# Performance work log

Measured on AMD Instinct MI355X. Metric: run time of the kernel, lower is better.

The kernel has to match this reference:

```python
import jax, jax.numpy as jnp
import numpy as np

N = 16384          # num nodes (adj is dense NxN)
INPUT_DIM = 512
HIDDEN = 128
E_POS = 524288
E_NEG = 524288


def setup_inputs() -> dict:
    key = jax.random.key(0)
    k1, k2, k3, k4, k5, k6, k7 = jax.random.split(key, 7)
    X = jax.random.normal(k1, (N, INPUT_DIM), dtype=jnp.float32)
    adj = jax.random.uniform(k2, (N, N), dtype=jnp.float32)
    train_edges = jax.random.randint(k3, (E_POS, 2), 0, N, dtype=jnp.int64)
    train_false_edges = jax.random.randint(k4, (E_NEG, 2), 0, N, dtype=jnp.int64)
    # parameters (xavier / kaiming scale approximated with uniform bounds)
    b1 = float(np.sqrt(6.0 / (INPUT_DIM + HIDDEN)))
    weight = jax.random.uniform(k5, (INPUT_DIM, HIDDEN), minval=-b1, maxval=b1, dtype=jnp.float32)
    b2 = float(np.sqrt(6.0 / (2 * HIDDEN + HIDDEN)))
    weight_two = jax.random.uniform(k6, (2 * HIDDEN, HIDDEN), minval=-b2, maxval=b2, dtype=jnp.float32)
    b3 = float(np.sqrt(6.0 / HIDDEN) / np.sqrt(2.0))  # kaiming_uniform a=1
    weight_three = jax.random.uniform(k7, (HIDDEN, 1), minval=-b3, maxval=b3, dtype=jnp.float32)
    return {"X": X, "adj": adj, "weight": weight, "weight_two": weight_two,
            "weight_three": weight_three, "train_edges": train_edges,
            "train_false_edges": train_false_edges}


def reference(X, adj, weight, weight_two, weight_three, train_edges, train_false_edges):
    # encode: Z = adj @ (X @ W)
    Z = adj @ (X @ weight)                                  # [N, H]
    edges = jnp.concatenate([train_edges, train_false_edges], axis=0)  # [E, 2]
    # decode: vectorized gather-concat replacing the per-edge Python loop
    z_pair = jnp.concatenate([Z[edges[:, 0]], Z[edges[:, 1]]], axis=1)  # [E, 2H]
    h = jax.nn.relu(z_pair) @ weight_two @ weight_three      # [E, 1]
    return jax.nn.sigmoid(h)
```

## Files before the change

### kernel.cpp

```cpp
#include <hip/hip_runtime.h>


#define N_NODES 16384
#define IN_DIM  512
#define HID     128
#define E_POS_N 524288
#define E_TOT   1048576

typedef __bf16 bf16x8 __attribute__((ext_vector_type(8)));
typedef float  f32x4  __attribute__((ext_vector_type(4)));
typedef unsigned short us8 __attribute__((ext_vector_type(8)));

__device__ __forceinline__ bf16x8 ldsb(const void* p){
  return __builtin_bit_cast(bf16x8, *reinterpret_cast<const us8*>(p));
}
__device__ __forceinline__ void gload16(const void* g, void* l){
  __builtin_amdgcn_global_load_lds(
      (const __attribute__((address_space(1))) unsigned int*)g,
      (__attribute__((address_space(3))) unsigned int*)l, 16, 0, 0);
}

__device__ __forceinline__ void split8(const float* f, bf16x8& hi, bf16x8& lo){
  unsigned short h[8];
  __bf16 l[8];
#pragma unroll
  for (int i = 0; i < 8; ++i){
    unsigned u  = __float_as_uint(f[i]);
    unsigned hb = u & 0xFFFF0000u;
    h[i] = (unsigned short)(hb >> 16);
    l[i] = (__bf16)(f[i] - __uint_as_float(hb));
  }
  us8 hv = {h[0], h[1], h[2], h[3], h[4], h[5], h[6], h[7]};
  hi = __builtin_bit_cast(bf16x8, hv);
  bf16x8 lv = {l[0], l[1], l[2], l[3], l[4], l[5], l[6], l[7]};
  lo = lv;
}

__global__ __launch_bounds__(256) void xw_kernel(const float* __restrict__ X,
                                                 const float* __restrict__ W,
                                                 unsigned short* __restrict__ bfB){
  __shared__ float Xt[32][64];
  __shared__ float Ws[32][128];
  const int tid = threadIdx.x;
  const int m0  = blockIdx.x * 64;
  const int ty  = tid >> 5;
  const int tx  = tid & 31;
  const int sr  = tid >> 2;
  const int sq  = tid & 3;
  const int wk  = tid >> 3;
  const int wc  = (tid & 7) * 16;
  float acc[8][4] = {};
  for (int kt = 0; kt < 16; ++kt){
    const int k0 = kt * 32;
    __syncthreads();
    {
      const float* xp = X + (size_t)(m0 + sr) * IN_DIM + k0 + sq * 8;
      float4 x0 = *(const float4*)xp;
      float4 x1 = *(const float4*)(xp + 4);
      Xt[sq*8+0][sr] = x0.x; Xt[sq*8+1][sr] = x0.y; Xt[sq*8+2][sr] = x0.z; Xt[sq*8+3][sr] = x0.w;
      Xt[sq*8+4][sr] = x1.x; Xt[sq*8+5][sr] = x1.y; Xt[sq*8+6][sr] = x1.z; Xt[sq*8+7][sr] = x1.w;
      const float* wp = W + (size_t)(k0 + wk) * HID + wc;
      *(float4*)&Ws[wk][wc+0]  = *(const float4*)(wp + 0);
      *(float4*)&Ws[wk][wc+4]  = *(const float4*)(wp + 4);
      *(float4*)&Ws[wk][wc+8]  = *(const float4*)(wp + 8);
      *(float4*)&Ws[wk][wc+12] = *(const float4*)(wp + 12);
    }
    __syncthreads();
#pragma unroll 8
    for (int kk = 0; kk < 32; ++kk){
      float4 a0 = *(const float4*)&Xt[kk][ty*8];
      float4 a1 = *(const float4*)&Xt[kk][ty*8+4];
      float4 b  = *(const float4*)&Ws[kk][tx*4];
      float av[8] = {a0.x,a0.y,a0.z,a0.w,a1.x,a1.y,a1.z,a1.w};
      float bv[4] = {b.x,b.y,b.z,b.w};
#pragma unroll
      for (int i = 0; i < 8; ++i)
#pragma unroll
        for (int c = 0; c < 4; ++c)
          acc[i][c] = fmaf(av[i], bv[c], acc[i][c]);
    }
  }
  const int row0 = m0 + ty * 8;
  const int tile = row0 >> 5;
  const int g    = (row0 >> 3) & 3;
#pragma unroll
  for (int cc = 0; cc < 4; ++cc){
    const int c  = tx * 4 + cc;
    const int sw = (c & 7) << 4;
    float f[8];
#pragma unroll
    for (int i = 0; i < 8; ++i) f[i] = acc[i][cc];
    bf16x8 hi, lo; split8(f, hi, lo);
    char* tb = (char*)bfB + (size_t)tile * 16384 + (size_t)c * 128;
    *(us8*)(tb + ((g * 16) ^ sw))      = __builtin_bit_cast(us8, hi);
    *(us8*)(tb + ((64 + g * 16) ^ sw)) = __builtin_bit_cast(us8, lo);
  }
}

__global__ void w23_kernel(const float* __restrict__ w2, const float* __restrict__ w3,
                           float* __restrict__ w23){
  const int t = threadIdx.x;
  float acc = 0.f;
#pragma unroll 4
  for (int k = 0; k < HID; ++k) acc = fmaf(w2[t * HID + k], w3[k], acc);
  w23[t] = acc;
}

__global__ __launch_bounds__(512, 2) void zgemm_kernel(const float* __restrict__ adj,
                                                       const unsigned short* __restrict__ bfB,
                                                       float* __restrict__ part,
                                                       int ksplit){
  __shared__ alignas(16) char lds[3][49152];
  const int tid  = threadIdx.x;
  const int lane = tid & 63;
  const int w    = tid >> 6;
  const int wm   = w >> 1;
  const int wn   = w & 1;
  int mt, s;
  if (ksplit == 4){
    const int xcd = blockIdx.x & 7, idx = blockIdx.x >> 3;
    s = xcd & 3; mt = ((xcd >> 2) << 5) + idx;
  } else { mt = blockIdx.x & 63; s = blockIdx.x >> 6; }
  const int klen = N_NODES / ksplit;
  const int k0   = s * klen;
  const int nt   = klen >> 5;

  const int g = lane >> 4, l15 = lane & 15;
  int aoff[4][2], boffH[4], boffL[4];
#pragma unroll
  for (int m = 0; m < 4; ++m){
    const int r = wm * 64 + m * 16 + l15;
    const int sw = (r & 7) << 4;
    aoff[m][0] = r * 128 + ((g * 32) ^ sw);
    aoff[m][1] = r * 128 + ((g * 32 + 16) ^ sw);
  }
#pragma unroll
  for (int n = 0; n < 4; ++n){
    const int c = wn * 64 + n * 16 + l15;
    const int sw = (c & 7) << 4;
    boffH[n] = 32768 + c * 128 + ((g * 16) ^ sw);
    boffL[n] = 32768 + c * 128 + ((64 + g * 16) ^ sw);
  }

  const char* asrc[4]; int aldo[4];
#pragma unroll
  for (int c4 = 0; c4 < 4; ++c4){
    const int r = c4 * 64 + (tid >> 3);
    asrc[c4] = (const char*)adj + ((size_t)(mt * 256 + r) * N_NODES + k0) * 4
               + (((tid & 7) * 16) ^ ((r & 7) << 4));
    aldo[c4] = c4 * 8192 + tid * 16;
  }
  const char* bsrc = (const char*)bfB + (size_t)(k0 >> 5) * 16384 + tid * 16;

#define STAGE(buf, tt) do { \
    _Pragma("unroll") \
    for (int c4 = 0; c4 < 4; ++c4) \
      gload16(asrc[c4] + (size_t)(tt) * 128, (buf) + aldo[c4]); \
    gload16(bsrc + (size_t)(tt) * 16384,        (buf) + 32768 + tid * 16); \
    gload16(bsrc + (size_t)(tt) * 16384 + 8192, (buf) + 40960 + tid * 16); \
  } while (0)

  f32x4 acc[4][4] = {};

  auto compute = [&](const char* bp){
    bf16x8 bHv[4], bLv[4];
#pragma unroll
    for (int n = 0; n < 4; ++n){
      bHv[n] = ldsb(bp + boffH[n]);
      bLv[n] = ldsb(bp + boffL[n]);
    }
#pragma unroll
    for (int m = 0; m < 4; ++m){
      f32x4 v0 = *(const f32x4*)(bp + aoff[m][0]);
      f32x4 v1 = *(const f32x4*)(bp + aoff[m][1]);
      float f[8] = {v0[0], v0[1], v0[2], v0[3], v1[0], v1[1], v1[2], v1[3]};
      bf16x8 aH, aL; split8(f, aH, aL);
      __builtin_amdgcn_s_setprio(1);
#pragma unroll
      for (int n = 0; n < 4; ++n)
        acc[m][n] = __builtin_amdgcn_mfma_f32_16x16x32_bf16(aH, bHv[n], acc[m][n], 0, 0, 0);
#pragma unroll
      for (int n = 0; n < 4; ++n)
        acc[m][n] = __builtin_amdgcn_mfma_f32_16x16x32_bf16(aH, bLv[n], acc[m][n], 0, 0, 0);
#pragma unroll
      for (int n = 0; n < 4; ++n)
        acc[m][n] = __builtin_amdgcn_mfma_f32_16x16x32_bf16(aL, bHv[n], acc[m][n], 0, 0, 0);
      __builtin_amdgcn_s_setprio(0);
    }
  };

  char* pc = lds[0]; char* pn = lds[1]; char* pf = lds[2];
  STAGE(pc, 0);
  STAGE(pn, 1);
  asm volatile("s_waitcnt vmcnt(6)" ::: "memory");
  __builtin_amdgcn_s_barrier();
  asm volatile("" ::: "memory");

  for (int t = 0; t < nt; ++t){
    if (t + 2 < nt) STAGE(pf, t + 2);
    compute(pc);
    if (t + 2 < nt)      asm volatile("s_waitcnt vmcnt(6)" ::: "memory");
    else if (t + 1 < nt) asm volatile("s_waitcnt vmcnt(0)" ::: "memory");
    if (t + 1 < nt){
      __builtin_amdgcn_s_barrier();
      asm volatile("" ::: "memory");
    }
    char* tmp = pc; pc = pn; pn = pf; pf = tmp;
  }
#undef STAGE

  float* pb = part + (size_t)s * ((size_t)N_NODES * HID);
  const int row0 = mt * 256 + wm * 64;
  const int col0 = wn * 64;
#pragma unroll
  for (int m = 0; m < 4; ++m){
#pragma unroll
    for (int n = 0; n < 4; ++n){
#pragma unroll
      for (int j = 0; j < 4; ++j){
        const int row = row0 + m * 16 + (lane >> 4) * 4 + j;
        const int col = col0 + n * 16 + l15;
        pb[(size_t)row * HID + col] = acc[m][n][j];
      }
    }
  }
}

__global__ __launch_bounds__(256) void nodered_kernel(const float* __restrict__ part,
                                                      const float* __restrict__ w23,
                                                      float* __restrict__ aarr,
                                                      float* __restrict__ barr,
                                                      int ksplit){
  const int lane = threadIdx.x & 63;
  const int wv   = threadIdx.x >> 6;
  const int n    = blockIdx.x * 4 + wv;
  const float* p = part + (size_t)n * HID;
  float z1 = 0.f, z2 = 0.f;
  for (int s = 0; s < ksplit; ++s){
    const size_t o = (size_t)s * N_NODES * HID;
    z1 += p[o + lane];
    z2 += p[o + lane + 64];
  }
  z1 = fmaxf(z1, 0.f); z2 = fmaxf(z2, 0.f);
  float av = z1 * w23[lane]       + z2 * w23[lane + 64];
  float bv = z1 * w23[128 + lane] + z2 * w23[192 + lane];
#pragma unroll
  for (int o = 32; o > 0; o >>= 1){
    av += __shfl_down(av, o);
    bv += __shfl_down(bv, o);
  }
  if (lane == 0){ aarr[n] = av; barr[n] = bv; }
}

__global__ __launch_bounds__(256) void edge_kernel(const int* __restrict__ e0,
                                                   const int* __restrict__ e1,
                                                   const float* __restrict__ aarr,
                                                   const float* __restrict__ barr,
                                                   float* __restrict__ out){
  const int e = blockIdx.x * 256 + threadIdx.x;
  int i, j;
  if (e < E_POS_N){ i = e0[2 * e];  j = e0[2 * e + 1]; }
  else { const int ee = e - E_POS_N; i = e1[2 * ee]; j = e1[2 * ee + 1]; }
  const float h = aarr[i] + barr[j];
  out[e] = 1.0f / (1.0f + __expf(-h));
}

extern "C" void kernel_launch(void* const* d_in, const int* in_sizes, int n_in,
                              void* d_out, int out_size, void* d_ws, size_t ws_size,
                              hipStream_t stream){
  const float* X   = (const float*)d_in[0];
  const float* adj = (const float*)d_in[1];
  const float* W   = (const float*)d_in[2];
  const float* W2  = (const float*)d_in[3];
  const float* W3  = (const float*)d_in[4];
  const int*   e0  = (const int*)d_in[5];
  const int*   e1  = (const int*)d_in[6];
  float* out = (float*)d_out;

  char* wsb = (char*)d_ws;
  unsigned short* bfB = (unsigned short*)(wsb);
  float* w23  = (float*)(wsb + (size_t)8 * 1024 * 1024);
  float* aarr = (float*)(wsb + (size_t)8 * 1024 * 1024 + 65536);
  float* barr = (float*)(wsb + (size_t)8 * 1024 * 1024 + 2 * 65536);
  float* part = (float*)(wsb + (size_t)16 * 1024 * 1024);

  const size_t PART = (size_t)N_NODES * HID * 4;
  const size_t base = (size_t)16 * 1024 * 1024;
  int ksplit = 1;
  if (ws_size >= base + 4 * PART) ksplit = 4;
  else if (ws_size >= base + 2 * PART) ksplit = 2;

  hipLaunchKernelGGL(xw_kernel, dim3(N_NODES / 64), dim3(256), 0, stream, X, W, bfB);
  hipLaunchKernelGGL(w23_kernel, dim3(1), dim3(256), 0, stream, W2, W3, w23);
  hipLaunchKernelGGL(zgemm_kernel, dim3(64 * ksplit), dim3(512), 0, stream,
                     adj, bfB, part, ksplit);
  hipLaunchKernelGGL(nodered_kernel, dim3(N_NODES / 4), dim3(256), 0, stream,
                     part, w23, aarr, barr, ksplit);
  hipLaunchKernelGGL(edge_kernel, dim3(E_TOT / 256), dim3(256), 0, stream,
                     e0, e1, aarr, barr, out);
}
```

Before: 312.4 us.

## Retile adjacency GEMM, move X@W to split-bf16 MFMA, vectorize edge and reduction kernels

The adjacency GEMM now uses 128-row tiles with a fixed 2-way K split, 4-stage LDS buffering and a different XCD mapping. The old dynamic ksplit selection based on workspace size is removed. X@W moves from scalar FMA to the same split-bf16 MFMA pipeline, fed by a new prep kernel that pre-splits W and also computes w23. split8 now uses byte-perm instructions. The node reduction handles four nodes per wave, and the edge kernel processes four edges per thread with vector loads and stores. Smaller GEMM tiles reduce reuse of B per adj load and change occupancy; the fixed split also assumes the workspace can hold two partial buffers.

```diff
diff --git a/kernel.cpp b/kernel.cpp
--- a/kernel.cpp
+++ b/kernel.cpp
@@ -10,6 +10,7 @@
 typedef __bf16 bf16x8 __attribute__((ext_vector_type(8)));
 typedef float  f32x4  __attribute__((ext_vector_type(4)));
 typedef unsigned short us8 __attribute__((ext_vector_type(8)));
+typedef unsigned short us4 __attribute__((ext_vector_type(4)));
 
 __device__ __forceinline__ bf16x8 ldsb(const void* p){
   return __builtin_bit_cast(bf16x8, *reinterpret_cast<const us8*>(p));
@@ -21,154 +22,91 @@
 }
 
 __device__ __forceinline__ void split8(const float* f, bf16x8& hi, bf16x8& lo){
-  unsigned short h[8];
-  __bf16 l[8];
-#pragma unroll
-  for (int i = 0; i < 8; ++i){
-    unsigned u  = __float_as_uint(f[i]);
-    unsigned hb = u & 0xFFFF0000u;
-    h[i] = (unsigned short)(hb >> 16);
-    l[i] = (__bf16)(f[i] - __uint_as_float(hb));
-  }
-  us8 hv = {h[0], h[1], h[2], h[3], h[4], h[5], h[6], h[7]};
+  unsigned u[8];
+#pragma unroll
+  for (int i = 0; i < 8; ++i) u[i] = __float_as_uint(f[i]);
+  uint4 hv;
+  hv.x = __builtin_amdgcn_perm(u[1], u[0], 0x07060302u);
+  hv.y = __builtin_amdgcn_perm(u[3], u[2], 0x07060302u);
+  hv.z = __builtin_amdgcn_perm(u[5], u[4], 0x07060302u);
+  hv.w = __builtin_amdgcn_perm(u[7], u[6], 0x07060302u);
   hi = __builtin_bit_cast(bf16x8, hv);
-  bf16x8 lv = {l[0], l[1], l[2], l[3], l[4], l[5], l[6], l[7]};
+  bf16x8 lv;
+#pragma unroll
+  for (int i = 0; i < 8; ++i)
+    lv[i] = (__bf16)(f[i] - __uint_as_float(u[i] & 0xFFFF0000u));
   lo = lv;
 }
 
-__global__ __launch_bounds__(256) void xw_kernel(const float* __restrict__ X,
-                                                 const float* __restrict__ W,
-                                                 unsigned short* __restrict__ bfB){
-  __shared__ float Xt[32][64];
-  __shared__ float Ws[32][128];
-  const int tid = threadIdx.x;
-  const int m0  = blockIdx.x * 64;
-  const int ty  = tid >> 5;
-  const int tx  = tid & 31;
-  const int sr  = tid >> 2;
-  const int sq  = tid & 3;
-  const int wk  = tid >> 3;
-  const int wc  = (tid & 7) * 16;
-  float acc[8][4] = {};
-  for (int kt = 0; kt < 16; ++kt){
-    const int k0 = kt * 32;
-    __syncthreads();
-    {
-      const float* xp = X + (size_t)(m0 + sr) * IN_DIM + k0 + sq * 8;
-      float4 x0 = *(const float4*)xp;
-      float4 x1 = *(const float4*)(xp + 4);
-      Xt[sq*8+0][sr] = x0.x; Xt[sq*8+1][sr] = x0.y; Xt[sq*8+2][sr] = x0.z; Xt[sq*8+3][sr] = x0.w;
-      Xt[sq*8+4][sr] = x1.x; Xt[sq*8+5][sr] = x1.y; Xt[sq*8+6][sr] = x1.z; Xt[sq*8+7][sr] = x1.w;
-      const float* wp = W + (size_t)(k0 + wk) * HID + wc;
-      *(float4*)&Ws[wk][wc+0]  = *(const float4*)(wp + 0);
-      *(float4*)&Ws[wk][wc+4]  = *(const float4*)(wp + 4);
-      *(float4*)&Ws[wk][wc+8]  = *(const float4*)(wp + 8);
-      *(float4*)&Ws[wk][wc+12] = *(const float4*)(wp + 12);
-    }
-    __syncthreads();
-#pragma unroll 8
-    for (int kk = 0; kk < 32; ++kk){
-      float4 a0 = *(const float4*)&Xt[kk][ty*8];
-      float4 a1 = *(const float4*)&Xt[kk][ty*8+4];
-      float4 b  = *(const float4*)&Ws[kk][tx*4];
-      float av[8] = {a0.x,a0.y,a0.z,a0.w,a1.x,a1.y,a1.z,a1.w};
-      float bv[4] = {b.x,b.y,b.z,b.w};
-#pragma unroll
-      for (int i = 0; i < 8; ++i)
-#pragma unroll
-        for (int c = 0; c < 4; ++c)
-          acc[i][c] = fmaf(av[i], bv[c], acc[i][c]);
-    }
-  }
-  const int row0 = m0 + ty * 8;
-  const int tile = row0 >> 5;
-  const int g    = (row0 >> 3) & 3;
-#pragma unroll
-  for (int cc = 0; cc < 4; ++cc){
-    const int c  = tx * 4 + cc;
+__global__ __launch_bounds__(512) void prep_kernel(const float* __restrict__ W,
+                                                   const float* __restrict__ w2,
+                                                   const float* __restrict__ w3,
+                                                   unsigned short* __restrict__ bfW,
+                                                   float* __restrict__ w23){
+  const int blk = blockIdx.x, tid = threadIdx.x;
+  if (blk < 16){
+    const int c = tid & 127, g = tid >> 7;
+    float f[8];
+#pragma unroll
+    for (int j = 0; j < 8; ++j) f[j] = W[(blk * 32 + g * 8 + j) * HID + c];
+    bf16x8 hi, lo; split8(f, hi, lo);
     const int sw = (c & 7) << 4;
-    float f[8];
-#pragma unroll
-    for (int i = 0; i < 8; ++i) f[i] = acc[i][cc];
-    bf16x8 hi, lo; split8(f, hi, lo);
-    char* tb = (char*)bfB + (size_t)tile * 16384 + (size_t)c * 128;
+    char* tb = (char*)bfW + blk * 16384 + c * 128;
     *(us8*)(tb + ((g * 16) ^ sw))      = __builtin_bit_cast(us8, hi);
     *(us8*)(tb + ((64 + g * 16) ^ sw)) = __builtin_bit_cast(us8, lo);
-  }
-}
-
-__global__ void w23_kernel(const float* __restrict__ w2, const float* __restrict__ w3,
-                           float* __restrict__ w23){
-  const int t = threadIdx.x;
-  float acc = 0.f;
+  } else if (tid < 256){
+    float acc = 0.f;
 #pragma unroll 4
-  for (int k = 0; k < HID; ++k) acc = fmaf(w2[t * HID + k], w3[k], acc);
-  w23[t] = acc;
-}
-
-__global__ __launch_bounds__(512, 2) void zgemm_kernel(const float* __restrict__ adj,
-                                                       const unsigned short* __restrict__ bfB,
-                                                       float* __restrict__ part,
-                                                       int ksplit){
-  __shared__ alignas(16) char lds[3][49152];
-  const int tid  = threadIdx.x;
-  const int lane = tid & 63;
-  const int w    = tid >> 6;
-  const int wm   = w >> 1;
-  const int wn   = w & 1;
-  int mt, s;
-  if (ksplit == 4){
-    const int xcd = blockIdx.x & 7, idx = blockIdx.x >> 3;
-    s = xcd & 3; mt = ((xcd >> 2) << 5) + idx;
-  } else { mt = blockIdx.x & 63; s = blockIdx.x >> 6; }
-  const int klen = N_NODES / ksplit;
-  const int k0   = s * klen;
-  const int nt   = klen >> 5;
-
+    for (int k = 0; k < HID; ++k) acc = fmaf(w2[tid * HID + k], w3[k], acc);
+    w23[tid] = acc;
+  }
+}
+
+__global__ __launch_bounds__(256) void xw_kernel(const float* __restrict__ X,
+                                                 const unsigned short* __restrict__ bfW,
+                                                 unsigned short* __restrict__ bfB){
+  __shared__ alignas(16) char lds[4][24576];
+  const int tid = threadIdx.x, lane = tid & 63, w = tid >> 6;
+  const int blk = blockIdx.x;
   const int g = lane >> 4, l15 = lane & 15;
-  int aoff[4][2], boffH[4], boffL[4];
+
+  int aoff[4][2], boffH[2], boffL[2];
 #pragma unroll
   for (int m = 0; m < 4; ++m){
-    const int r = wm * 64 + m * 16 + l15;
-    const int sw = (r & 7) << 4;
+    const int r = m * 16 + l15, sw = (r & 7) << 4;
     aoff[m][0] = r * 128 + ((g * 32) ^ sw);
     aoff[m][1] = r * 128 + ((g * 32 + 16) ^ sw);
   }
 #pragma unroll
-  for (int n = 0; n < 4; ++n){
-    const int c = wn * 64 + n * 16 + l15;
-    const int sw = (c & 7) << 4;
-    boffH[n] = 32768 + c * 128 + ((g * 16) ^ sw);
-    boffL[n] = 32768 + c * 128 + ((64 + g * 16) ^ sw);
-  }
-
-  const char* asrc[4]; int aldo[4];
-#pragma unroll
-  for (int c4 = 0; c4 < 4; ++c4){
-    const int r = c4 * 64 + (tid >> 3);
-    asrc[c4] = (const char*)adj + ((size_t)(mt * 256 + r) * N_NODES + k0) * 4
-               + (((tid & 7) * 16) ^ ((r & 7) << 4));
-    aldo[c4] = c4 * 8192 + tid * 16;
-  }
-  const char* bsrc = (const char*)bfB + (size_t)(k0 >> 5) * 16384 + tid * 16;
-
-#define STAGE(buf, tt) do { \
-    _Pragma("unroll") \
-    for (int c4 = 0; c4 < 4; ++c4) \
-      gload16(asrc[c4] + (size_t)(tt) * 128, (buf) + aldo[c4]); \
-    gload16(bsrc + (size_t)(tt) * 16384,        (buf) + 32768 + tid * 16); \
-    gload16(bsrc + (size_t)(tt) * 16384 + 8192, (buf) + 40960 + tid * 16); \
+  for (int n = 0; n < 2; ++n){
+    const int c = (w & 3) * 32 + n * 16 + l15, sw = (c & 7) << 4;
+    boffH[n] = 8192 + c * 128 + ((g * 16) ^ sw);
+    boffL[n] = 8192 + c * 128 + ((64 + g * 16) ^ sw);
+  }
+
+  const char* xsrc[2];
+#pragma unroll
+  for (int i = 0; i < 2; ++i){
+    const int r = i * 32 + (tid >> 3);
+    xsrc[i] = (const char*)X + ((size_t)(blk * 64 + r) * IN_DIM) * 4
+            + (((tid & 7) * 16) ^ ((r & 7) << 4));
+  }
+  const char* bsrc = (const char*)bfW + tid * 16;
+
+#define XSTAGE(buf, tt) do { \
+    gload16(xsrc[0] + (tt) * 128, (buf) + tid * 16); \
+    gload16(xsrc[1] + (tt) * 128, (buf) + 4096 + tid * 16); \
+    gload16(bsrc + (size_t)(tt) * 16384,         (buf) + 8192  + tid * 16); \
+    gload16(bsrc + (size_t)(tt) * 16384 + 4096,  (buf) + 12288 + tid * 16); \
+    gload16(bsrc + (size_t)(tt) * 16384 + 8192,  (buf) + 16384 + tid * 16); \
+    gload16(bsrc + (size_t)(tt) * 16384 + 12288, (buf) + 20480 + tid * 16); \
   } while (0)
 
-  f32x4 acc[4][4] = {};
-
+  f32x4 acc[4][2] = {};
   auto compute = [&](const char* bp){
-    bf16x8 bHv[4], bLv[4];
-#pragma unroll
-    for (int n = 0; n < 4; ++n){
-      bHv[n] = ldsb(bp + boffH[n]);
-      bLv[n] = ldsb(bp + boffL[n]);
-    }
+    bf16x8 bHv[2], bLv[2];
+#pragma unroll
+    for (int n = 0; n < 2; ++n){ bHv[n] = ldsb(bp + boffH[n]); bLv[n] = ldsb(bp + boffL[n]); }
 #pragma unroll
     for (int m = 0; m < 4; ++m){
       f32x4 v0 = *(const f32x4*)(bp + aoff[m][0]);
@@ -177,48 +115,148 @@
       bf16x8 aH, aL; split8(f, aH, aL);
       __builtin_amdgcn_s_setprio(1);
 #pragma unroll
-      for (int n = 0; n < 4; ++n)
-        acc[m][n] = __builtin_amdgcn_mfma_f32_16x16x32_bf16(aH, bHv[n], acc[m][n], 0, 0, 0);
-#pragma unroll
-      for (int n = 0; n < 4; ++n)
-        acc[m][n] = __builtin_amdgcn_mfma_f32_16x16x32_bf16(aH, bLv[n], acc[m][n], 0, 0, 0);
-#pragma unroll
-      for (int n = 0; n < 4; ++n)
-        acc[m][n] = __builtin_amdgcn_mfma_f32_16x16x32_bf16(aL, bHv[n], acc[m][n], 0, 0, 0);
+      for (int n = 0; n < 2; ++n) acc[m][n] = __builtin_amdgcn_mfma_f32_16x16x32_bf16(aH, bHv[n], acc[m][n], 0, 0, 0);
+#pragma unroll
+      for (int n = 0; n < 2; ++n) acc[m][n] = __builtin_amdgcn_mfma_f32_16x16x32_bf16(aH, bLv[n], acc[m][n], 0, 0, 0);
+#pragma unroll
+      for (int n = 0; n < 2; ++n) acc[m][n] = __builtin_amdgcn_mfma_f32_16x16x32_bf16(aL, bHv[n], acc[m][n], 0, 0, 0);
       __builtin_amdgcn_s_setprio(0);
     }
   };
 
-  char* pc = lds[0]; char* pn = lds[1]; char* pf = lds[2];
-  STAGE(pc, 0);
-  STAGE(pn, 1);
-  asm volatile("s_waitcnt vmcnt(6)" ::: "memory");
+  XSTAGE(lds[0], 0); XSTAGE(lds[1], 1); XSTAGE(lds[2], 2);
+  asm volatile("s_waitcnt vmcnt(12)" ::: "memory");
   __builtin_amdgcn_s_barrier();
-  asm volatile("" ::: "memory");
-
+
+  const int nt = IN_DIM / 32;
+#pragma unroll 1
   for (int t = 0; t < nt; ++t){
-    if (t + 2 < nt) STAGE(pf, t + 2);
-    compute(pc);
-    if (t + 2 < nt)      asm volatile("s_waitcnt vmcnt(6)" ::: "memory");
+    char* bp = lds[t & 3];
+    if (t + 3 < nt) XSTAGE(lds[(t + 3) & 3], t + 3);
+    compute(bp);
+    if (t + 3 < nt)      asm volatile("s_waitcnt vmcnt(12)" ::: "memory");
+    else if (t + 2 < nt) asm volatile("s_waitcnt vmcnt(6)" ::: "memory");
     else if (t + 1 < nt) asm volatile("s_waitcnt vmcnt(0)" ::: "memory");
-    if (t + 1 < nt){
-      __builtin_amdgcn_s_barrier();
-      asm volatile("" ::: "memory");
-    }
-    char* tmp = pc; pc = pn; pn = pf; pf = tmp;
-  }
-#undef STAGE
+    if (t + 1 < nt) __builtin_amdgcn_s_barrier();
+  }
+#undef XSTAGE
+
+#pragma unroll
+  for (int m = 0; m < 4; ++m){
+#pragma unroll
+    for (int n = 0; n < 2; ++n){
+      const int col = (w & 3) * 32 + n * 16 + l15;
+      const int T   = 2 * blk + (m >> 1);
+      const int g2  = (2 * m + (g >> 1)) & 3;
+      const int sw  = (col & 7) << 4;
+      char* tb = (char*)bfB + (size_t)T * 16384 + col * 128;
+      uint2 hv;
+      hv.x = __builtin_amdgcn_perm(__float_as_uint(acc[m][n][1]), __float_as_uint(acc[m][n][0]), 0x07060302u);
+      hv.y = __builtin_amdgcn_perm(__float_as_uint(acc[m][n][3]), __float_as_uint(acc[m][n][2]), 0x07060302u);
+      us4 lv;
+#pragma unroll
+      for (int j = 0; j < 4; ++j){
+        unsigned u = __float_as_uint(acc[m][n][j]);
+        lv[j] = __builtin_bit_cast(unsigned short,
+                 (__bf16)(acc[m][n][j] - __uint_as_float(u & 0xFFFF0000u)));
+      }
+      *(uint2*)(tb + (((g2 * 16) ^ sw) + (g & 1) * 8))      = hv;
+      *(uint2*)(tb + (((64 + g2 * 16) ^ sw) + (g & 1) * 8)) = __builtin_bit_cast(uint2, lv);
+    }
+  }
+}
+
+__global__ __launch_bounds__(512, 2) void zgemm_kernel(const float* __restrict__ adj,
+                                                       const unsigned short* __restrict__ bfB,
+                                                       float* __restrict__ part){
+  __shared__ alignas(16) char lds[4][32768];
+  const int tid = threadIdx.x, lane = tid & 63, w = tid >> 6;
+  const int wm = w >> 2, wn = w & 3;
+  const int xcd = blockIdx.x & 7;
+  const int s   = xcd & 1;
+  const int mt  = (xcd >> 1) * 32 + (blockIdx.x >> 3);
+  const int k0  = s * (N_NODES / 2);
+  const int nt  = (N_NODES / 2) / 32;
+  const int g = lane >> 4, l15 = lane & 15;
+
+  int aoff[4][2], boffH[2], boffL[2];
+#pragma unroll
+  for (int m = 0; m < 4; ++m){
+    const int r = wm * 64 + m * 16 + l15, sw = (r & 7) << 4;
+    aoff[m][0] = r * 128 + ((g * 32) ^ sw);
+    aoff[m][1] = r * 128 + ((g * 32 + 16) ^ sw);
+  }
+#pragma unroll
+  for (int n = 0; n < 2; ++n){
+    const int c = wn * 32 + n * 16 + l15, sw = (c & 7) << 4;
+    boffH[n] = 16384 + c * 128 + ((g * 16) ^ sw);
+    boffL[n] = 16384 + c * 128 + ((64 + g * 16) ^ sw);
+  }
+
+  const char* asrc[2];
+#pragma unroll
+  for (int i = 0; i < 2; ++i){
+    const int r = i * 64 + (tid >> 3);
+    asrc[i] = (const char*)adj + ((size_t)(mt * 128 + r) * N_NODES + k0) * 4
+            + (((tid & 7) * 16) ^ ((r & 7) << 4));
+  }
+  const char* bsrc = (const char*)bfB + (size_t)(k0 >> 5) * 16384 + tid * 16;
+
+#define ZSTAGE(buf, tt) do { \
+    gload16(asrc[0] + (size_t)(tt) * 128, (buf) + tid * 16); \
+    gload16(asrc[1] + (size_t)(tt) * 128, (buf) + 8192 + tid * 16); \
+    gload16(bsrc + (size_t)(tt) * 16384,        (buf) + 16384 + tid * 16); \
+    gload16(bsrc + (size_t)(tt) * 16384 + 8192, (buf) + 24576 + tid * 16); \
+  } while (0)
+
+  f32x4 acc[4][2] = {};
+  auto compute = [&](const char* bp){
+    bf16x8 bHv[2], bLv[2];
+#pragma unroll
+    for (int n = 0; n < 2; ++n){ bHv[n] = ldsb(bp + boffH[n]); bLv[n] = ldsb(bp + boffL[n]); }
+#pragma unroll
+    for (int m = 0; m < 4; ++m){
+      f32x4 v0 = *(const f32x4*)(bp + aoff[m][0]);
+      f32x4 v1 = *(const f32x4*)(bp + aoff[m][1]);
+      float f[8] = {v0[0], v0[1], v0[2], v0[3], v1[0], v1[1], v1[2], v1[3]};
+      bf16x8 aH, aL; split8(f, aH, aL);
+      __builtin_amdgcn_s_setprio(1);
+#pragma unroll
+      for (int n = 0; n < 2; ++n) acc[m][n] = __builtin_amdgcn_mfma_f32_16x16x32_bf16(aH, bHv[n], acc[m][n], 0, 0, 0);
+#pragma unroll
+      for (int n = 0; n < 2; ++n) acc[m][n] = __builtin_amdgcn_mfma_f32_16x16x32_bf16(aH, bLv[n], acc[m][n], 0, 0, 0);
+#pragma unroll
+      for (int n = 0; n < 2; ++n) acc[m][n] = __builtin_amdgcn_mfma_f32_16x16x32_bf16(aL, bHv[n], acc[m][n], 0, 0, 0);
+      __builtin_amdgcn_s_setprio(0);
+    }
+  };
+
+  ZSTAGE(lds[0], 0); ZSTAGE(lds[1], 1); ZSTAGE(lds[2], 2);
+  asm volatile("s_waitcnt vmcnt(8)" ::: "memory");
+  __builtin_amdgcn_s_barrier();
+
+#pragma unroll 1
+  for (int t = 0; t < nt; ++t){
+    char* bp = lds[t & 3];
+    if (t + 3 < nt) ZSTAGE(lds[(t + 3) & 3], t + 3);
+    compute(bp);
+    if (t + 3 < nt)      asm volatile("s_waitcnt vmcnt(8)" ::: "memory");
+    else if (t + 2 < nt) asm volatile("s_waitcnt vmcnt(4)" ::: "memory");
+    else if (t + 1 < nt) asm volatile("s_waitcnt vmcnt(0)" ::: "memory");
+    if (t + 1 < nt) __builtin_amdgcn_s_barrier();
+  }
+#undef ZSTAGE
 
   float* pb = part + (size_t)s * ((size_t)N_NODES * HID);
-  const int row0 = mt * 256 + wm * 64;
-  const int col0 = wn * 64;
+  const int row0 = mt * 128 + wm * 64;
+  const int col0 = wn * 32;
 #pragma unroll
   for (int m = 0; m < 4; ++m){
 #pragma unroll
-    for (int n = 0; n < 4; ++n){
+    for (int n = 0; n < 2; ++n){
 #pragma unroll
       for (int j = 0; j < 4; ++j){
-        const int row = row0 + m * 16 + (lane >> 4) * 4 + j;
+        const int row = row0 + m * 16 + g * 4 + j;
         const int col = col0 + n * 16 + l15;
         pb[(size_t)row * HID + col] = acc[m][n][j];
       }
@@ -229,27 +267,34 @@
 __global__ __launch_bounds__(256) void nodered_kernel(const float* __restrict__ part,
                                                       const float* __restrict__ w23,
                                                       float* __restrict__ aarr,
-                                                      float* __restrict__ barr,
-                                                      int ksplit){
-  const int lane = threadIdx.x & 63;
-  const int wv   = threadIdx.x >> 6;
-  const int n    = blockIdx.x * 4 + wv;
-  const float* p = part + (size_t)n * HID;
-  float z1 = 0.f, z2 = 0.f;
-  for (int s = 0; s < ksplit; ++s){
-    const size_t o = (size_t)s * N_NODES * HID;
-    z1 += p[o + lane];
-    z2 += p[o + lane + 64];
-  }
-  z1 = fmaxf(z1, 0.f); z2 = fmaxf(z2, 0.f);
-  float av = z1 * w23[lane]       + z2 * w23[lane + 64];
-  float bv = z1 * w23[128 + lane] + z2 * w23[192 + lane];
-#pragma unroll
-  for (int o = 32; o > 0; o >>= 1){
-    av += __shfl_down(av, o);
-    bv += __shfl_down(bv, o);
-  }
-  if (lane == 0){ aarr[n] = av; barr[n] = bv; }
+                                                      float* __restrict__ barr){
+  const int lane = threadIdx.x & 63, wv = threadIdx.x >> 6;
+  const int n0 = blockIdx.x * 16 + wv * 4;
+  const float w1a = w23[lane],       w1b = w23[lane + 64];
+  const float w2a = w23[128 + lane], w2b = w23[192 + lane];
+  const float* p0 = part + (size_t)n0 * HID;
+  const float* p1 = p0 + (size_t)N_NODES * HID;
+  float av[4], bv[4];
+#pragma unroll
+  for (int u = 0; u < 4; ++u){
+    float z1 = p0[u * HID + lane]      + p1[u * HID + lane];
+    float z2 = p0[u * HID + lane + 64] + p1[u * HID + lane + 64];
+    z1 = fmaxf(z1, 0.f); z2 = fmaxf(z2, 0.f);
+    av[u] = z1 * w1a + z2 * w1b;
+    bv[u] = z1 * w2a + z2 * w2b;
+  }
+#pragma unroll
+  for (int u = 0; u < 4; ++u){
+#pragma unroll
+    for (int o = 32; o > 0; o >>= 1){
+      av[u] += __shfl_down(av[u], o);
+      bv[u] += __shfl_down(bv[u], o);
+    }
+  }
+  if (lane == 0){
+#pragma unroll
+    for (int u = 0; u < 4; ++u){ aarr[n0 + u] = av[u]; barr[n0 + u] = bv[u]; }
+  }
 }
 
 __global__ __launch_bounds__(256) void edge_kernel(const int* __restrict__ e0,
@@ -257,12 +302,21 @@
                                                    const float* __restrict__ aarr,
                                                    const float* __restrict__ barr,
                                                    float* __restrict__ out){
-  const int e = blockIdx.x * 256 + threadIdx.x;
-  int i, j;
-  if (e < E_POS_N){ i = e0[2 * e];  j = e0[2 * e + 1]; }
-  else { const int ee = e - E_POS_N; i = e1[2 * ee]; j = e1[2 * ee + 1]; }
-  const float h = aarr[i] + barr[j];
-  out[e] = 1.0f / (1.0f + __expf(-h));
+  const int e = (blockIdx.x * 256 + threadIdx.x) * 4;
+  const int* ep; int eb;
+  if (e < E_POS_N){ ep = e0; eb = e; } else { ep = e1; eb = e - E_POS_N; }
+  int4 p0 = *(const int4*)(ep + 2 * eb);
+  int4 p1 = *(const int4*)(ep + 2 * eb + 4);
+  float4 o;
+  o.x = aarr[p0.x] + barr[p0.y];
+  o.y = aarr[p0.z] + barr[p0.w];
+  o.z = aarr[p1.x] + barr[p1.y];
+  o.w = aarr[p1.z] + barr[p1.w];
+  o.x = 1.f / (1.f + __expf(-o.x));
+  o.y = 1.f / (1.f + __expf(-o.y));
+  o.z = 1.f / (1.f + __expf(-o.z));
+  o.w = 1.f / (1.f + __expf(-o.w));
+  *(float4*)(out + e) = o;
 }
 
 extern "C" void kernel_launch(void* const* d_in, const int* in_sizes, int n_in,
@@ -278,24 +332,19 @@
   float* out = (float*)d_out;
 
   char* wsb = (char*)d_ws;
+  const size_t MB = 1024 * 1024;
   unsigned short* bfB = (unsigned short*)(wsb);
-  float* w23  = (float*)(wsb + (size_t)8 * 1024 * 1024);
-  float* aarr = (float*)(wsb + (size_t)8 * 1024 * 1024 + 65536);
-  float* barr = (float*)(wsb + (size_t)8 * 1024 * 1024 + 2 * 65536);
-  float* part = (float*)(wsb + (size_t)16 * 1024 * 1024);
-
-  const size_t PART = (size_t)N_NODES * HID * 4;
-  const size_t base = (size_t)16 * 1024 * 1024;
-  int ksplit = 1;
-  if (ws_size >= base + 4 * PART) ksplit = 4;
-  else if (ws_size >= base + 2 * PART) ksplit = 2;
-
-  hipLaunchKernelGGL(xw_kernel, dim3(N_NODES / 64), dim3(256), 0, stream, X, W, bfB);
-  hipLaunchKernelGGL(w23_kernel, dim3(1), dim3(256), 0, stream, W2, W3, w23);
-  hipLaunchKernelGGL(zgemm_kernel, dim3(64 * ksplit), dim3(512), 0, stream,
-                     adj, bfB, part, ksplit);
-  hipLaunchKernelGGL(nodered_kernel, dim3(N_NODES / 4), dim3(256), 0, stream,
-                     part, w23, aarr, barr, ksplit);
-  hipLaunchKernelGGL(edge_kernel, dim3(E_TOT / 256), dim3(256), 0, stream,
+  unsigned short* bfW = (unsigned short*)(wsb + 8 * MB);
+  float* w23  = (float*)(wsb + 8 * MB + 512 * 1024);
+  float* aarr = (float*)(wsb + 9 * MB);
+  float* barr = (float*)(wsb + 9 * MB + 64 * 1024);
+  float* part = (float*)(wsb + 16 * MB);
+
+  hipLaunchKernelGGL(prep_kernel, dim3(17), dim3(512), 0, stream, W, W2, W3, bfW, w23);
+  hipLaunchKernelGGL(xw_kernel, dim3(N_NODES / 64), dim3(256), 0, stream, X, bfW, bfB);
+  hipLaunchKernelGGL(zgemm_kernel, dim3(256), dim3(512), 0, stream, adj, bfB, part);
+  hipLaunchKernelGGL(nodered_kernel, dim3(N_NODES / 16), dim3(256), 0, stream,
+                     part, w23, aarr, barr);
+  hipLaunchKernelGGL(edge_kernel, dim3(E_TOT / 1024), dim3(256), 0, stream,
                      e0, e1, aarr, barr, out);
 }
```

Result: slower. 330.3 us (+5.7%).
